# Kernel tuning notes

Measured on AMD Instinct MI355X. Metric: run time of the kernel, lower is better.

The kernel has to match this reference:

```python
import jax, jax.numpy as jnp
import numpy as np

B, T, E, H, K = 128, 199, 256, 256, 8  # batch, max_step-1, embed, hidden, hist_neighbor_num


def setup_inputs() -> dict:
    key = jax.random.key(0)
    ks = jax.random.split(key, 14)
    f = lambda i, shape, s=1.0: jax.random.normal(ks[i], shape, dtype=jnp.float32) * s
    w = 0.05  # weight init scale
    return {
        'input_questions_embedding': f(0, (B, T, E)),
        'next_questions_embedding': f(1, (B, T, E)),
        'input_skills_embedding': f(2, (B, T, E)),
        'input_answers_embedding': f(3, (B, T, E)),
        'hist_neighbor_index': jax.random.randint(ks[4], (B, T, K), 0, T),
        # next_feature_linear (E -> H)
        'W_next_feat': f(5, (H, E), w), 'b_next_feat': jnp.zeros((H,), jnp.float32),
        # lstm_input_embedding (3E -> H)
        'W_lstm_in': f(6, (H, 3 * E), w), 'b_lstm_in': jnp.zeros((H,), jnp.float32),
        # single-layer LSTM (torch gate order i,f,g,o)
        'W_ih': f(7, (4 * H, H), w), 'W_hh': f(8, (4 * H, H), w),
        'b_ih': jnp.zeros((4 * H,), jnp.float32), 'b_hh': jnp.zeros((4 * H,), jnp.float32),
        # attention1 / attention2 (H -> 1)
        'att1_w': f(9, (H, 1), w), 'att1_b': jnp.zeros((1,), jnp.float32),
        'att2_w': f(10, (H, 1), w), 'att2_b': jnp.zeros((1,), jnp.float32),
    }


def _lstm(x, W_ih, W_hh, b_ih, b_hh):
    # x: [B,T,H_in] -> outputs [B,T,H]; torch nn.LSTM gate order (i, f, g, o)
    hsz = W_hh.shape[1]
    bsz = x.shape[0]
    xp = jnp.einsum('btd,gd->tbg', x, W_ih) + b_ih  # precompute input projection [T,B,4H]

    def step(carry, xt):
        h, c = carry
        gates = xt + h @ W_hh.T + b_hh
        i, f, g, o = jnp.split(gates, 4, axis=-1)
        c = jax.nn.sigmoid(f) * c + jax.nn.sigmoid(i) * jnp.tanh(g)
        h = jax.nn.sigmoid(o) * jnp.tanh(c)
        return (h, c), h

    init = (jnp.zeros((bsz, hsz), x.dtype), jnp.zeros((bsz, hsz), x.dtype))
    _, hs = jax.lax.scan(step, init, xp)  # [T,B,H]
    return hs.transpose(1, 0, 2)


def reference(input_questions_embedding, next_questions_embedding,
              input_skills_embedding, input_answers_embedding,
              hist_neighbor_index,
              W_next_feat, b_next_feat, W_lstm_in, b_lstm_in,
              W_ih, W_hh, b_ih, b_hh,
              att1_w, att1_b, att2_w, att2_b):
    bsz, t = input_questions_embedding.shape[0], input_questions_embedding.shape[1]
    # next question representation: linear + relu  [B,T,H]
    next_trans = jax.nn.relu(jnp.einsum('bte,he->bth', next_questions_embedding, W_next_feat) + b_next_feat)
    # LSTM input: concat(question, answer, skill) -> linear  [B,T,H]
    fa = jnp.concatenate([input_questions_embedding, input_answers_embedding, input_skills_embedding], axis=-1)
    x_in = jnp.einsum('btd,hd->bth', fa, W_lstm_in) + b_lstm_in
    # knowledge-state series (dropout is identity at inference)
    output_series = _lstm(x_in, W_ih, W_hh, b_ih, b_hh)  # [B,T,H]
    # hard history-neighbor sampler: gather K past states per (b,t)  [B,T,K,H]
    hist = output_series[jnp.arange(bsz)[:, None, None], hist_neighbor_index]
    Nh = jnp.concatenate([output_series[:, :, None, :], hist], axis=2)  # [B,T,K+1,H]
    Nn = next_trans[:, :, None, :]  # [B,T,1,H]  (next_neighbor_num == 0)
    # pairwise interactions
    logits = jnp.einsum('btkh,btnh->btkn', Nh, Nn).reshape(bsz, t, -1)  # [B,T,(K+1)*1]
    f1 = Nh @ att1_w + att1_b  # [B,T,K+1,1]
    f2 = Nn @ att2_w + att2_b  # [B,T,1,1]
    coefs = jax.nn.softmax(jnp.tanh((f1 + f2).reshape(bsz, t, -1)), axis=2)
    return jnp.sum(logits * coefs, axis=-1)  # [B,T]
```

## Files before the change

### kernel.cpp

```cpp
#include <hip/hip_runtime.h>
#include <hip/hip_bf16.h>
#include <stdint.h>

#define DEV __device__ __forceinline__

typedef __bf16 bf16;
typedef __attribute__((ext_vector_type(8))) __bf16 bf16x8;
typedef __attribute__((ext_vector_type(4))) float f32x4;
typedef __attribute__((ext_vector_type(4))) unsigned short u16x4;

constexpr int Bb = 128, Tt = 199, Ee = 256, Hh = 256;
constexpr int Mm = Bb * Tt;
constexpr int G4 = 4 * Hh;

constexpr size_t OFF_FLAGS = 0;
constexpr size_t OFF_WLI_H = 8192;
constexpr size_t OFF_WLI_L = OFF_WLI_H + (size_t)Hh * 768 * 2;
constexpr size_t OFF_WIH_H = OFF_WLI_L + (size_t)Hh * 768 * 2;
constexpr size_t OFF_WIH_L = OFF_WIH_H + (size_t)G4 * Hh * 2;
constexpr size_t OFF_WNF_H = OFF_WIH_L + (size_t)G4 * Hh * 2;
constexpr size_t OFF_WNF_L = OFF_WNF_H + (size_t)Hh * Ee * 2;
constexpr size_t OFF_WHB   = OFF_WNF_L + (size_t)Hh * Ee * 2;
constexpr size_t OFF_XIN_H = OFF_WHB   + (size_t)G4 * Hh * 2;
constexpr size_t OFF_XIN_L = OFF_XIN_H + (size_t)Mm * Hh * 2;
constexpr size_t OFF_XPH   = OFF_XIN_L + (size_t)Mm * Hh * 2;
constexpr size_t OFF_HEX   = OFF_XPH   + (size_t)Mm * G4 * 2;
constexpr size_t OFF_NTR   = OFF_HEX   + (size_t)Mm * Hh * 4;
constexpr size_t WS_NEED   = OFF_NTR   + (size_t)Mm * Hh * 4;

DEV float sigm(float x)  { return 1.0f / (1.0f + __expf(-x)); }
DEV float tanh_(float x) { return 2.0f / (1.0f + __expf(-2.0f * x)) - 1.0f; }
DEV float b2f(unsigned short u) { return __uint_as_float(((unsigned)u) << 16); }
DEV unsigned short f2bbits(bf16 h) { union { bf16 b; unsigned short u; } cv; cv.b = h; return cv.u; }

#define MFMA16(a, b, c) __builtin_amdgcn_mfma_f32_16x16x32_bf16(a, b, c, 0, 0, 0)

__global__ void k_reset(unsigned int* flags) {
    int i = blockIdx.x * 256 + threadIdx.x;
    if (i < 32 * 16) flags[i] = 0;
}

__global__ void k_prep(const float* __restrict__ Wli, const float* __restrict__ Wih,
                       const float* __restrict__ Wnf, const float* __restrict__ Whh,
                       bf16* wli_h, bf16* wli_l, bf16* wih_h, bf16* wih_l,
                       bf16* wnf_h, bf16* wnf_l, bf16* whb) {
    const int n1 = Hh * 768, n2 = G4 * Hh, n3 = Hh * Ee, n4 = G4 * Hh;
    const int ntot = n1 + n2 + n3 + n4;
    for (int idx = blockIdx.x * 256 + threadIdx.x; idx < ntot; idx += gridDim.x * 256) {
        if (idx < n1 + n2 + n3) {
            const float* src; bf16 *dh, *dl; int j;
            if (idx < n1)           { src = Wli; dh = wli_h; dl = wli_l; j = idx; }
            else if (idx < n1 + n2) { src = Wih; dh = wih_h; dl = wih_l; j = idx - n1; }
            else                    { src = Wnf; dh = wnf_h; dl = wnf_l; j = idx - n1 - n2; }
            float x = src[j];
            bf16 h = (bf16)x;
            dh[j] = h;
            dl[j] = (bf16)(x - (float)h);
        } else {
            int j = idx - n1 - n2 - n3;
            whb[j] = (bf16)Whh[j];
        }
    }
}

template<int AMODE, int EPI, int KT, int NTOT>
__global__ __launch_bounds__(256, 2)
void k_gemm(const float* __restrict__ a0, const float* __restrict__ a1,
            const float* __restrict__ a2,
            const bf16* __restrict__ ah_src, const bf16* __restrict__ al_src,
            const bf16* __restrict__ bh_src, const bf16* __restrict__ bl_src,
            const float* __restrict__ bias0, const float* __restrict__ bias1,
            float* __restrict__ outf, bf16* __restrict__ outh, bf16* __restrict__ outl)
{
    __shared__ __align__(16) bf16 lA[2][128 * 64];
    __shared__ __align__(16) bf16 lB[2][128 * 64];
    const int tid = threadIdx.x;
    const int l = tid & 63, w = tid >> 6;
    const int wr = w >> 1, wc = w & 1;
    const int lr = l & 15, lh = l >> 4;
    const int mb = blockIdx.x;
    const int nb = blockIdx.y;

    f32x4 acc[4][4];
    #pragma unroll
    for (int i = 0; i < 4; ++i)
        #pragma unroll
        for (int j = 0; j < 4; ++j) acc[i][j] = {};

    for (int ks = 0; ks < KT / 64; ++ks) {
        #pragma unroll
        for (int p = 0; p < 4; ++p) {
            int Gi = p * 256 + tid;
            int row = Gi >> 3, gsl = Gi & 7;
            int k = ks * 64 + gsl * 8;
            int dst = row * 64 + ((gsl ^ (row & 7)) * 8);
            if constexpr (AMODE == 2) {
                size_t base = (size_t)(mb * 128 + row) * KT + k;
                *(bf16x8*)&lA[0][dst] = *(const bf16x8*)(ah_src + base);
                *(bf16x8*)&lA[1][dst] = *(const bf16x8*)(al_src + base);
            } else {
                const float* src; int e;
                if constexpr (AMODE == 0) {
                    int seg = k >> 8; e = k & 255;
                    src = (seg == 0) ? a0 : (seg == 1) ? a1 : a2;
                } else { src = a0; e = k; }
                size_t base = ((size_t)row * Tt + mb) * Ee + e;
                float4 v0 = *(const float4*)(src + base);
                float4 v1 = *(const float4*)(src + base + 4);
                float vv[8] = {v0.x, v0.y, v0.z, v0.w, v1.x, v1.y, v1.z, v1.w};
                bf16x8 hv, lv;
                #pragma unroll
                for (int j = 0; j < 8; ++j) {
                    bf16 h = (bf16)vv[j];
                    hv[j] = h;
                    lv[j] = (bf16)(vv[j] - (float)h);
                }
                *(bf16x8*)&lA[0][dst] = hv;
                *(bf16x8*)&lA[1][dst] = lv;
            }
            size_t bbase = (size_t)(nb * 128 + row) * KT + k;
            *(bf16x8*)&lB[0][dst] = *(const bf16x8*)(bh_src + bbase);
            *(bf16x8*)&lB[1][dst] = *(const bf16x8*)(bl_src + bbase);
        }
        __syncthreads();
        #pragma unroll
        for (int kt = 0; kt < 2; ++kt) {
            bf16x8 ah[4], al[4], bh[4], bl[4];
            #pragma unroll
            for (int mt = 0; mt < 4; ++mt) {
                int row = wr * 64 + mt * 16 + lr;
                int g = (kt * 4 + lh) ^ (row & 7);
                ah[mt] = *(const bf16x8*)&lA[0][row * 64 + g * 8];
                al[mt] = *(const bf16x8*)&lA[1][row * 64 + g * 8];
            }
            #pragma unroll
            for (int nt = 0; nt < 4; ++nt) {
                int row = wc * 64 + nt * 16 + lr;
                int g = (kt * 4 + lh) ^ (row & 7);
                bh[nt] = *(const bf16x8*)&lB[0][row * 64 + g * 8];
                bl[nt] = *(const bf16x8*)&lB[1][row * 64 + g * 8];
            }
            #pragma unroll
            for (int mt = 0; mt < 4; ++mt)
                #pragma unroll
                for (int nt = 0; nt < 4; ++nt) {
                    acc[mt][nt] = MFMA16(ah[mt], bh[nt], acc[mt][nt]);
                    acc[mt][nt] = MFMA16(ah[mt], bl[nt], acc[mt][nt]);
                    acc[mt][nt] = MFMA16(al[mt], bh[nt], acc[mt][nt]);
                }
        }
        __syncthreads();
    }
    if constexpr (EPI == 1) {
        #pragma unroll
        for (int nt = 0; nt < 4; ++nt) {
            int n = nb * 128 + wc * 64 + nt * 16 + lr;
            float bv = bias0[n] + bias1[n];
            #pragma unroll
            for (int mt = 0; mt < 4; ++mt) {
                int bq = wr * 4 + mt;
                u16x4 pk;
                #pragma unroll
                for (int r = 0; r < 4; ++r)
                    pk[r] = f2bbits((bf16)(acc[mt][nt][r] + bv));
                *(u16x4*)(outh + (((size_t)mb * 8 + bq) * 1024 + n) * 16 + lh * 4) = pk;
            }
        }
    } else {
        #pragma unroll
        for (int nt = 0; nt < 4; ++nt) {
            int n = nb * 128 + wc * 64 + nt * 16 + lr;
            float bv = bias0[n];
            #pragma unroll
            for (int mt = 0; mt < 4; ++mt)
                #pragma unroll
                for (int r = 0; r < 4; ++r) {
                    int m = mb * 128 + wr * 64 + mt * 16 + lh * 4 + r;
                    float v = acc[mt][nt][r] + bv;
                    if constexpr (EPI == 0) {
                        bf16 h = (bf16)v;
                        outh[(size_t)m * NTOT + n] = h;
                        outl[(size_t)m * NTOT + n] = (bf16)(v - (float)h);
                    } else {
                        outf[(size_t)m * NTOT + n] = fmaxf(v, 0.f);
                    }
                }
        }
    }
}

__global__ __launch_bounds__(256, 1)
void k_lstm(const bf16* __restrict__ whb, const bf16* __restrict__ xph,
            float* __restrict__ hexch, unsigned int* __restrict__ flags)
{
    __shared__ __align__(16) bf16 hstage[16 * 256];
    const int tid = threadIdx.x;
    const int l = tid & 63, w = tid >> 6;
    const int lr = l & 15, lh = l >> 4;
    const int g = blockIdx.x & 7;
    const int c = blockIdx.x >> 3;

    const int ju = c * 64 + w * 16 + lr;

    f32x4 wf[4][8];
    #pragma unroll
    for (int q = 0; q < 4; ++q)
        #pragma unroll
        for (int kt = 0; kt < 8; ++kt)
            wf[q][kt] = *(const f32x4*)(whb + (size_t)(q * 256 + ju) * 256 + kt * 32 + lh * 8);

    unsigned int* selfflag = flags + (g * 4 + c) * 16;
    f32x4 cst = {};

    for (int t = 0; t < Tt; ++t) {
        f32x4 acc[4] = {};
        u16x4 xq[4];
        const bf16* xb = xph + (size_t)(t * 8 + g) * 1024 * 16;

        if (t > 0) {
            if (l < 4 && l != c) {
                const unsigned int* fp = flags + (g * 4 + l) * 16;
                while (__hip_atomic_load(fp, __ATOMIC_RELAXED, __HIP_MEMORY_SCOPE_AGENT) < (unsigned)t)
                    __builtin_amdgcn_s_sleep(1);
            }
            asm volatile("" ::: "memory");

            {
                int m = tid >> 4, j0 = (tid & 15) * 16;
                const float* hp = hexch + ((size_t)(g * Tt + (t - 1)) * 16 + m) * 256 + j0;
                union { unsigned long long u[8]; float f[16]; } hv;
                #pragma unroll
                for (int jj = 0; jj < 8; ++jj)
                    hv.u[jj] = __hip_atomic_load((const unsigned long long*)(hp + jj * 2),
                                                 __ATOMIC_RELAXED, __HIP_MEMORY_SCOPE_AGENT);
                bf16x8 p0, p1;
                #pragma unroll
                for (int jj = 0; jj < 8; ++jj) { p0[jj] = (bf16)hv.f[jj]; p1[jj] = (bf16)hv.f[8 + jj]; }
                int gk0 = j0 >> 3;
                *(bf16x8*)&hstage[m * 256 + (((gk0)     + m) & 31) * 8] = p0;
                *(bf16x8*)&hstage[m * 256 + (((gk0 + 1) + m) & 31) * 8] = p1;
            }
            asm volatile("s_waitcnt lgkmcnt(0)\n\ts_barrier" ::: "memory");

            #pragma unroll
            for (int kt = 0; kt < 8; ++kt) {
                bf16x8 af = *(const bf16x8*)&hstage[lr * 256 + ((kt * 4 + lh + lr) & 31) * 8];
                if (kt == 4) {
                    #pragma unroll
                    for (int q = 0; q < 4; ++q)
                        xq[q] = *(const u16x4*)(xb + (size_t)(q * 256 + ju) * 16 + lh * 4);
                }
                #pragma unroll
                for (int q = 0; q < 4; ++q)
                    acc[q] = MFMA16(af, __builtin_bit_cast(bf16x8, wf[q][kt]), acc[q]);
            }
        } else {
            #pragma unroll
            for (int q = 0; q < 4; ++q)
                xq[q] = *(const u16x4*)(xb + (size_t)(q * 256 + ju) * 16 + lh * 4);
        }

        float* hg = hexch + (size_t)(g * Tt + t) * 16 * 256;
        #pragma unroll
        for (int r = 0; r < 4; ++r) {
            float iv = acc[0][r] + b2f(xq[0][r]);
            float fv = acc[1][r] + b2f(xq[1][r]);
            float gv = acc[2][r] + b2f(xq[2][r]);
            float ov = acc[3][r] + b2f(xq[3][r]);
            float cn = sigm(fv) * cst[r] + sigm(iv) * tanh_(gv);
            cst[r] = cn;
            float hv = sigm(ov) * tanh_(cn);
            int m = lh * 4 + r;
            __hip_atomic_store(hg + (size_t)m * 256 + ju, hv,
                               __ATOMIC_RELAXED, __HIP_MEMORY_SCOPE_AGENT);
        }
        asm volatile("s_waitcnt vmcnt(0)" ::: "memory");
        __syncthreads();
        if (tid == 0)
            __hip_atomic_fetch_add(selfflag, 1u, __ATOMIC_RELAXED, __HIP_MEMORY_SCOPE_AGENT);
    }
}

DEV float wred(float v) {
    #pragma unroll
    for (int off = 32; off > 0; off >>= 1) v += __shfl_down(v, off, 64);
    return v;
}

__global__ __launch_bounds__(256, 4)
void k_attn(const float* __restrict__ hexch, const float* __restrict__ ntr,
            const int* __restrict__ hidx,
            const float* __restrict__ a1w, const float* __restrict__ a1b,
            const float* __restrict__ a2w, const float* __restrict__ a2b,
            float* __restrict__ out)
{
    int wid = blockIdx.x * 4 + (threadIdx.x >> 6);
    if (wid >= Mm) return;
    int l = threadIdx.x & 63;
    int t = wid / Bb, b = wid % Bb;
    int g = b >> 4, bi = b & 15;

    float4 nt4 = *(const float4*)(ntr + (size_t)wid * 256 + l * 4);
    float4 w14 = *(const float4*)(a1w + l * 4);
    float4 w24 = *(const float4*)(a2w + l * 4);
    float lg[9], fh[9];
    float fn = nt4.x * w24.x + nt4.y * w24.y + nt4.z * w24.z + nt4.w * w24.w;
    #pragma unroll
    for (int k = 0; k < 9; ++k) {
        int ts = (k == 0) ? t : hidx[((size_t)b * Tt + t) * 8 + (k - 1)];
        const float* hrow = hexch + ((size_t)(g * Tt + ts) * 16 + bi) * 256;
        float4 h4 = *(const float4*)(hrow + l * 4);
        lg[k] = h4.x * nt4.x + h4.y * nt4.y + h4.z * nt4.z + h4.w * nt4.w;
        fh[k] = h4.x * w14.x + h4.y * w14.y + h4.z * w14.z + h4.w * w14.w;
    }
    #pragma unroll
    for (int k = 0; k < 9; ++k) { lg[k] = wred(lg[k]); fh[k] = wred(fh[k]); }
    fn = wred(fn);
    if (l == 0) {
        float f2 = fn + a2b[0], b1 = a1b[0];
        float tv[9], mx = -1e30f;
        #pragma unroll
        for (int k = 0; k < 9; ++k) { tv[k] = tanh_(fh[k] + b1 + f2); mx = fmaxf(mx, tv[k]); }
        float s = 0.f, accv = 0.f;
        #pragma unroll
        for (int k = 0; k < 9; ++k) { float e = __expf(tv[k] - mx); s += e; accv += e * lg[k]; }
        out[(size_t)b * Tt + t] = accv / s;
    }
}

extern "C" void kernel_launch(void* const* d_in, const int* in_sizes, int n_in,
                              void* d_out, int out_size, void* d_ws, size_t ws_size,
                              hipStream_t stream)
{
    const float* q   = (const float*)d_in[0];
    const float* nq  = (const float*)d_in[1];
    const float* sk  = (const float*)d_in[2];
    const float* an  = (const float*)d_in[3];
    const int*   hid = (const int*)d_in[4];
    const float* Wnf = (const float*)d_in[5];
    const float* bnf = (const float*)d_in[6];
    const float* Wli = (const float*)d_in[7];
    const float* bli = (const float*)d_in[8];
    const float* Wih = (const float*)d_in[9];
    const float* Whh = (const float*)d_in[10];
    const float* bih = (const float*)d_in[11];
    const float* bhh = (const float*)d_in[12];
    const float* a1w = (const float*)d_in[13];
    const float* a1b = (const float*)d_in[14];
    const float* a2w = (const float*)d_in[15];
    const float* a2b = (const float*)d_in[16];
    float* out = (float*)d_out;

    char* ws = (char*)d_ws;
    unsigned int* flags = (unsigned int*)(ws + OFF_FLAGS);
    bf16* wli_h = (bf16*)(ws + OFF_WLI_H);
    bf16* wli_l = (bf16*)(ws + OFF_WLI_L);
    bf16* wih_h = (bf16*)(ws + OFF_WIH_H);
    bf16* wih_l = (bf16*)(ws + OFF_WIH_L);
    bf16* wnf_h = (bf16*)(ws + OFF_WNF_H);
    bf16* wnf_l = (bf16*)(ws + OFF_WNF_L);
    bf16* whb   = (bf16*)(ws + OFF_WHB);
    bf16* xin_h = (bf16*)(ws + OFF_XIN_H);
    bf16* xin_l = (bf16*)(ws + OFF_XIN_L);
    bf16* xph   = (bf16*)(ws + OFF_XPH);
    float* hex  = (float*)(ws + OFF_HEX);
    float* ntr  = (float*)(ws + OFF_NTR);

    k_reset<<<2, 256, 0, stream>>>(flags);
    k_prep<<<512, 256, 0, stream>>>(Wli, Wih, Wnf, Whh, wli_h, wli_l, wih_h, wih_l,
                                    wnf_h, wnf_l, whb);

    dim3 g1(Tt, 2);
    k_gemm<0, 0, 768, 256><<<g1, 256, 0, stream>>>(q, an, sk, nullptr, nullptr,
        wli_h, wli_l, bli, nullptr, nullptr, xin_h, xin_l);

    dim3 g2(Tt, 8);
    k_gemm<2, 1, 256, 1024><<<g2, 256, 0, stream>>>(nullptr, nullptr, nullptr, xin_h, xin_l,
        wih_h, wih_l, bih, bhh, nullptr, xph, nullptr);

    dim3 g3(Tt, 2);
    k_gemm<1, 2, 256, 256><<<g3, 256, 0, stream>>>(nq, nullptr, nullptr, nullptr, nullptr,
        wnf_h, wnf_l, bnf, nullptr, ntr, nullptr, nullptr);

    k_lstm<<<32, 256, 0, stream>>>(whb, xph, hex, flags);

    k_attn<<<Mm / 4, 256, 0, stream>>>(hex, ntr, hid, a1w, a1b, a2w, a2b, out);
    (void)in_sizes; (void)n_in; (void)out_size; (void)ws_size;
}
```

Before: 809.2 us.

## Exchange LSTM hidden state as bf16 with per-wave flags and no LDS staging

The recurrent LSTM kernel now publishes each step's hidden state to a separate bf16 buffer. Consumers load it straight from global memory into MFMA operands instead of converting fp32 into LDS and hitting a block barrier. Signalling moves from one flag per block with __syncthreads to one flag per wave, set with a plain store, so each wave only waits on the 16 producer waves of its group. The fp32 copy needed by attention is written after the flag, taking it off the critical path. This cuts per-step latency on the serial recurrence, but adds more flag polling and uncoalesced global loads of the operands.

```diff
diff --git a/kernel.cpp b/kernel.cpp
--- a/kernel.cpp
+++ b/kernel.cpp
@@ -14,7 +14,7 @@
 constexpr int G4 = 4 * Hh;
 
 constexpr size_t OFF_FLAGS = 0;
-constexpr size_t OFF_WLI_H = 8192;
+constexpr size_t OFF_WLI_H = 16384;
 constexpr size_t OFF_WLI_L = OFF_WLI_H + (size_t)Hh * 768 * 2;
 constexpr size_t OFF_WIH_H = OFF_WLI_L + (size_t)Hh * 768 * 2;
 constexpr size_t OFF_WIH_L = OFF_WIH_H + (size_t)G4 * Hh * 2;
@@ -25,7 +25,8 @@
 constexpr size_t OFF_XIN_L = OFF_XIN_H + (size_t)Mm * Hh * 2;
 constexpr size_t OFF_XPH   = OFF_XIN_L + (size_t)Mm * Hh * 2;
 constexpr size_t OFF_HEX   = OFF_XPH   + (size_t)Mm * G4 * 2;
-constexpr size_t OFF_NTR   = OFF_HEX   + (size_t)Mm * Hh * 4;
+constexpr size_t OFF_HMB   = OFF_HEX   + (size_t)Mm * Hh * 4;
+constexpr size_t OFF_NTR   = OFF_HMB   + (size_t)Mm * Hh * 2;
 constexpr size_t WS_NEED   = OFF_NTR   + (size_t)Mm * Hh * 4;
 
 DEV float sigm(float x)  { return 1.0f / (1.0f + __expf(-x)); }
@@ -37,7 +38,7 @@
 
 __global__ void k_reset(unsigned int* flags) {
     int i = blockIdx.x * 256 + threadIdx.x;
-    if (i < 32 * 16) flags[i] = 0;
+    if (i < 128 * 16) flags[i] = 0;
 }
 
 __global__ void k_prep(const float* __restrict__ Wli, const float* __restrict__ Wih,
@@ -191,9 +192,9 @@
 
 __global__ __launch_bounds__(256, 1)
 void k_lstm(const bf16* __restrict__ whb, const bf16* __restrict__ xph,
-            float* __restrict__ hexch, unsigned int* __restrict__ flags)
+            float* __restrict__ hexch, bf16* __restrict__ hmb,
+            unsigned int* __restrict__ flags)
 {
-    __shared__ __align__(16) bf16 hstage[16 * 256];
     const int tid = threadIdx.x;
     const int l = tid & 63, w = tid >> 6;
     const int lr = l & 15, lh = l >> 4;
@@ -209,58 +210,43 @@
         for (int kt = 0; kt < 8; ++kt)
             wf[q][kt] = *(const f32x4*)(whb + (size_t)(q * 256 + ju) * 256 + kt * 32 + lh * 8);
 
-    unsigned int* selfflag = flags + (g * 4 + c) * 16;
+    unsigned int* selfflag = flags + ((size_t)(g * 4 + c) * 4 + w) * 16;
     f32x4 cst = {};
 
     for (int t = 0; t < Tt; ++t) {
+        const bf16* xb = xph + (size_t)(t * 8 + g) * 1024 * 16;
+        u16x4 xq[4];
+        #pragma unroll
+        for (int q = 0; q < 4; ++q)
+            xq[q] = *(const u16x4*)(xb + (size_t)(q * 256 + ju) * 16 + lh * 4);
+
         f32x4 acc[4] = {};
-        u16x4 xq[4];
-        const bf16* xb = xph + (size_t)(t * 8 + g) * 1024 * 16;
 
         if (t > 0) {
-            if (l < 4 && l != c) {
-                const unsigned int* fp = flags + (g * 4 + l) * 16;
+            if (l < 16) {
+                const unsigned int* fp = flags + (size_t)(g * 16 + l) * 16;
                 while (__hip_atomic_load(fp, __ATOMIC_RELAXED, __HIP_MEMORY_SCOPE_AGENT) < (unsigned)t)
                     __builtin_amdgcn_s_sleep(1);
             }
             asm volatile("" ::: "memory");
 
-            {
-                int m = tid >> 4, j0 = (tid & 15) * 16;
-                const float* hp = hexch + ((size_t)(g * Tt + (t - 1)) * 16 + m) * 256 + j0;
-                union { unsigned long long u[8]; float f[16]; } hv;
-                #pragma unroll
-                for (int jj = 0; jj < 8; ++jj)
-                    hv.u[jj] = __hip_atomic_load((const unsigned long long*)(hp + jj * 2),
-                                                 __ATOMIC_RELAXED, __HIP_MEMORY_SCOPE_AGENT);
-                bf16x8 p0, p1;
-                #pragma unroll
-                for (int jj = 0; jj < 8; ++jj) { p0[jj] = (bf16)hv.f[jj]; p1[jj] = (bf16)hv.f[8 + jj]; }
-                int gk0 = j0 >> 3;
-                *(bf16x8*)&hstage[m * 256 + (((gk0)     + m) & 31) * 8] = p0;
-                *(bf16x8*)&hstage[m * 256 + (((gk0 + 1) + m) & 31) * 8] = p1;
-            }
-            asm volatile("s_waitcnt lgkmcnt(0)\n\ts_barrier" ::: "memory");
-
+            const bf16* mb = hmb + (size_t)(g * Tt + (t - 1)) * 16 * 256;
             #pragma unroll
             for (int kt = 0; kt < 8; ++kt) {
-                bf16x8 af = *(const bf16x8*)&hstage[lr * 256 + ((kt * 4 + lh + lr) & 31) * 8];
-                if (kt == 4) {
-                    #pragma unroll
-                    for (int q = 0; q < 4; ++q)
-                        xq[q] = *(const u16x4*)(xb + (size_t)(q * 256 + ju) * 16 + lh * 4);
-                }
+                const unsigned long long* ap =
+                    (const unsigned long long*)(mb + lr * 256 + kt * 32 + lh * 8);
+                union { unsigned long long u[2]; bf16x8 v; } cv;
+                cv.u[0] = __hip_atomic_load(ap,     __ATOMIC_RELAXED, __HIP_MEMORY_SCOPE_AGENT);
+                cv.u[1] = __hip_atomic_load(ap + 1, __ATOMIC_RELAXED, __HIP_MEMORY_SCOPE_AGENT);
+                bf16x8 af = cv.v;
                 #pragma unroll
                 for (int q = 0; q < 4; ++q)
                     acc[q] = MFMA16(af, __builtin_bit_cast(bf16x8, wf[q][kt]), acc[q]);
             }
-        } else {
-            #pragma unroll
-            for (int q = 0; q < 4; ++q)
-                xq[q] = *(const u16x4*)(xb + (size_t)(q * 256 + ju) * 16 + lh * 4);
-        }
-
-        float* hg = hexch + (size_t)(g * Tt + t) * 16 * 256;
+        }
+
+        bf16* mbw = hmb + (size_t)(g * Tt + t) * 16 * 256;
+        float hv4[4];
         #pragma unroll
         for (int r = 0; r < 4; ++r) {
             float iv = acc[0][r] + b2f(xq[0][r]);
@@ -270,14 +256,21 @@
             float cn = sigm(fv) * cst[r] + sigm(iv) * tanh_(gv);
             cst[r] = cn;
             float hv = sigm(ov) * tanh_(cn);
+            hv4[r] = hv;
             int m = lh * 4 + r;
-            __hip_atomic_store(hg + (size_t)m * 256 + ju, hv,
+            __hip_atomic_store((unsigned short*)(mbw + (size_t)m * 256 + ju),
+                               f2bbits((bf16)hv),
                                __ATOMIC_RELAXED, __HIP_MEMORY_SCOPE_AGENT);
         }
         asm volatile("s_waitcnt vmcnt(0)" ::: "memory");
-        __syncthreads();
-        if (tid == 0)
-            __hip_atomic_fetch_add(selfflag, 1u, __ATOMIC_RELAXED, __HIP_MEMORY_SCOPE_AGENT);
+        if (l == 0)
+            __hip_atomic_store(selfflag, (unsigned)(t + 1),
+                               __ATOMIC_RELAXED, __HIP_MEMORY_SCOPE_AGENT);
+
+        float* hg = hexch + (size_t)(g * Tt + t) * 16 * 256;
+        #pragma unroll
+        for (int r = 0; r < 4; ++r)
+            hg[(size_t)(lh * 4 + r) * 256 + ju] = hv4[r];
     }
 }
 
@@ -364,9 +357,10 @@
     bf16* xin_l = (bf16*)(ws + OFF_XIN_L);
     bf16* xph   = (bf16*)(ws + OFF_XPH);
     float* hex  = (float*)(ws + OFF_HEX);
+    bf16* hmb   = (bf16*)(ws + OFF_HMB);
     float* ntr  = (float*)(ws + OFF_NTR);
 
-    k_reset<<<2, 256, 0, stream>>>(flags);
+    k_reset<<<8, 256, 0, stream>>>(flags);
     k_prep<<<512, 256, 0, stream>>>(Wli, Wih, Wnf, Whh, wli_h, wli_l, wih_h, wih_l,
                                     wnf_h, wnf_l, whb);
 
@@ -382,7 +376,7 @@
     k_gemm<1, 2, 256, 256><<<g3, 256, 0, stream>>>(nq, nullptr, nullptr, nullptr, nullptr,
         wnf_h, wnf_l, bnf, nullptr, ntr, nullptr, nullptr);
 
-    k_lstm<<<32, 256, 0, stream>>>(whb, xph, hex, flags);
+    k_lstm<<<32, 256, 0, stream>>>(whb, xph, hex, hmb, flags);
 
     k_attn<<<Mm / 4, 256, 0, stream>>>(hex, ntr, hid, a1w, a1b, a2w, a2b, out);
     (void)in_sizes; (void)n_in; (void)out_size; (void)ws_size;
```

Result: slower. 1.023 ms (+26.5%).
